# Kernel optimization log

Hardware: AMD Instinct MI355X
Metric: run time of the kernel (lower is better)

Reference implementation:

```python
import jax, jax.numpy as jnp
import numpy as np

B, L, N, H, D, TOPK = 32, 720, 512, 16, 64, 8
TEMP = 1.0


def setup_inputs() -> dict:
    key = jax.random.key(0)
    ks = jax.random.split(key, 18)
    s = lambda k, shp, fan: jax.random.normal(k, shp, jnp.float32) / np.sqrt(fan)
    return {
        'x': jax.random.normal(ks[0], (B, L, N), jnp.float32),
        'var_embed': s(ks[1], (N, H), H),
        'Wq': s(ks[2], (H, H), H), 'bq': jnp.zeros((H,), jnp.float32),
        'Wk': s(ks[3], (H, H), H), 'bk': jnp.zeros((H,), jnp.float32),
        'Wscore': s(ks[4], (N, 1), N), 'bscore': jnp.zeros((1,), jnp.float32),
        'Wc1': s(ks[5], (N, D), N), 'bc1': jnp.zeros((D,), jnp.float32),
        'Wc2': s(ks[6], (D, D), D), 'bc2': jnp.zeros((D,), jnp.float32),
        'Wcn': s(ks[7], (D, N), D), 'bcn': jnp.zeros((N,), jnp.float32),
        'Wg': s(ks[8], (2 * N, N), 2 * N), 'bg': jnp.zeros((N,), jnp.float32),
        'Wf': s(ks[9], (N, N), N), 'bf': jnp.zeros((N,), jnp.float32),
        'gamma': jnp.ones((N,), jnp.float32), 'beta': jnp.zeros((N,), jnp.float32),
    }


def _forward(x, var_embed, Wq, bq, Wk, bk, Wscore, bscore, Wc1, bc1, Wc2, bc2,
             Wcn, bcn, Wg, bg, Wf, bf, gamma, beta):
    # --- SparseVariableRouter (eval mode: no gumbel noise) ---
    Q = var_embed @ Wq + bq          # [N,H]
    K = var_embed @ Wk + bk          # [N,H]
    sim = Q @ K.T                    # [N,N] (identical across batch in torch)
    eye = jnp.eye(N, dtype=bool)
    sim = jnp.where(eye, -1e9, sim)
    topk_vals, topk_idx = jax.lax.top_k(sim, TOPK)      # [N,k]
    w = jax.nn.softmax(topk_vals / TEMP, axis=-1)        # [N,k]
    x_perm = jnp.transpose(x, (0, 2, 1))                 # [B,N,L]
    neighbors = x_perm[:, topk_idx, :]                   # [B,N,k,L] gather
    ring_out = jnp.einsum('bnkl,nk->bln', neighbors, w)  # [B,L,N]
    # --- center path ---
    attn = jax.nn.softmax(x @ Wscore + bscore, axis=1)   # [B,L,1] softmax over L
    center_raw = jnp.sum(x * attn, axis=1)               # [B,N]
    c = jax.nn.gelu(center_raw @ Wc1 + bc1, approximate=False)
    c = jax.nn.gelu(c @ Wc2 + bc2, approximate=False)
    center = c @ Wcn + bcn                               # [B,N]
    center_b = jnp.broadcast_to(center[:, None, :], (x.shape[0], x.shape[1], N))
    # --- gated fusion + residual LN ---
    gate = jax.nn.sigmoid(jnp.concatenate([ring_out, center_b], axis=-1) @ Wg + bg)
    fused = gate * ring_out + (1.0 - gate) * center_b
    fused = fused @ Wf + bf
    h = fused + x
    mu = jnp.mean(h, axis=-1, keepdims=True)
    var = jnp.var(h, axis=-1, keepdims=True)
    return (h - mu) * jax.lax.rsqrt(var + 1e-5) * gamma + beta


def reference(x, var_embed, Wq, bq, Wk, bk, Wscore, bscore, Wc1, bc1, Wc2, bc2,
              Wcn, bcn, Wg, bg, Wf, bf, gamma, beta):
    return _forward(x, var_embed, Wq, bq, Wk, bk, Wscore, bscore, Wc1, bc1,
                    Wc2, bc2, Wcn, bcn, Wg, bg, Wf, bf, gamma, beta)
```

## Files before the change

kernel.cpp:

```cpp
#include <hip/hip_runtime.h>
#include <hip/hip_bf16.h>
#include <math.h>

#define B_ 32
#define L_ 720
#define N_ 512
#define H_ 16
#define D_ 64
#define TOPK_ 8
#define M_ (B_ * L_)
#define RPB 8
#define CRCH 16
#define CRL (L_ / CRCH)
#define OROWS 64

typedef __bf16 bf16x8 __attribute__((ext_vector_type(8)));
typedef float f32x16 __attribute__((ext_vector_type(16)));

__device__ __forceinline__ void async_cp16(const __hip_bfloat16* g, __hip_bfloat16* l) {
    __builtin_amdgcn_global_load_lds(
        (const __attribute__((address_space(1))) void*)g,
        (__attribute__((address_space(3))) void*)l, 16, 0, 0);
}

__device__ __forceinline__ bf16x8 frag_ld(const __hip_bfloat16* base, int row, int j0) {
    return *(const bf16x8*)(base + row * 64 + (((j0) ^ (row & 7)) << 3));
}

__device__ __forceinline__ f32x16 fzero16() {
    f32x16 z;
    #pragma unroll
    for (int e = 0; e < 16; ++e) z[e] = 0.f;
    return z;
}

__global__ __launch_bounds__(512) void prep_kernel(
    const float* __restrict__ Wg, const float* __restrict__ Wf,
    __hip_bfloat16* __restrict__ WgT, __hip_bfloat16* __restrict__ WfT,
    const float* __restrict__ ve,
    const float* __restrict__ Wq, const float* __restrict__ bq,
    const float* __restrict__ Wk, const float* __restrict__ bk,
    float* __restrict__ Qm, float* __restrict__ Km)
{
    const int bx = blockIdx.x;
    if (bx < 512) {
        const int n = bx;
        const int k = threadIdx.x;
        WgT[n * N_ + k] = __float2bfloat16(Wg[(size_t)k * N_ + n]);
        WfT[n * N_ + k] = __float2bfloat16(Wf[(size_t)k * N_ + n]);
    } else {
        const int g = (bx - 512) * 512 + threadIdx.x;
        const int j = g >> 4, h = g & 15;
        const float* vr = ve + j * H_;
        float q = bq[h], k = bk[h];
        #pragma unroll
        for (int m = 0; m < H_; ++m) {
            const float v = vr[m];
            q += v * Wq[m * H_ + h];
            k += v * Wk[m * H_ + h];
        }
        Qm[g] = q;
        Km[g] = k;
    }
}

__global__ __launch_bounds__(64) void topk_kernel(
    const float* __restrict__ Qm, const float* __restrict__ Km,
    float* __restrict__ w_out, int* __restrict__ idx_out)
{
    const int n = blockIdx.x;
    const int lane = threadIdx.x;

    float4 q0, q1, q2, q3;
    {
        const float4* qr = (const float4*)(Qm + n * H_);
        q0 = qr[0]; q1 = qr[1]; q2 = qr[2]; q3 = qr[3];
    }

    float sv[8]; int si[8];
    #pragma unroll
    for (int c = 0; c < 8; ++c) {
        const int j = c * 64 + lane;
        const float4* kr = (const float4*)(Km + j * H_);
        float4 k0 = kr[0], k1 = kr[1], k2 = kr[2], k3 = kr[3];
        float s = q0.x * k0.x + q0.y * k0.y + q0.z * k0.z + q0.w * k0.w
                + q1.x * k1.x + q1.y * k1.y + q1.z * k1.z + q1.w * k1.w
                + q2.x * k2.x + q2.y * k2.y + q2.z * k2.z + q2.w * k2.w
                + q3.x * k3.x + q3.y * k3.y + q3.z * k3.z + q3.w * k3.w;
        sv[c] = (j == n) ? -1e9f : s;
        si[c] = j;
    }

    float keepv[TOPK_]; int keepi[TOPK_];
    #pragma unroll
    for (int k = 0; k < TOPK_; ++k) {
        float bv = sv[0]; int bi = si[0]; int bslot = 0;
        #pragma unroll
        for (int c = 1; c < 8; ++c)
            if (sv[c] > bv || (sv[c] == bv && si[c] < bi)) { bv = sv[c]; bi = si[c]; bslot = c; }
        float v = bv; int i = bi;
        #pragma unroll
        for (int off = 32; off > 0; off >>= 1) {
            float v2 = __shfl_xor(v, off);
            int   i2 = __shfl_xor(i, off);
            if (v2 > v || (v2 == v && i2 < i)) { v = v2; i = i2; }
        }
        keepv[k] = v; keepi[k] = i;
        if (i == bi) sv[bslot] = -INFINITY;
    }

    if (lane == 0) {
        float vmax = keepv[0];
        float ev[TOPK_], esum = 0.f;
        #pragma unroll
        for (int k = 0; k < TOPK_; k++) { ev[k] = expf(keepv[k] - vmax); esum += ev[k]; }
        float inv = 1.f / esum;
        #pragma unroll
        for (int k = 0; k < TOPK_; k++) {
            w_out[n * TOPK_ + k] = ev[k] * inv;
            idx_out[n * TOPK_ + k] = keepi[k];
        }
    }
}

__global__ __launch_bounds__(512) void ring_kernel(
    const float* __restrict__ x, const float* __restrict__ w,
    const int* __restrict__ idx,
    const float* __restrict__ Wscore, const float* __restrict__ bscore,
    __hip_bfloat16* __restrict__ ring, float* __restrict__ s)
{
    __shared__ float xs[RPB][N_];
    __shared__ float wsh[N_ * TOPK_];
    __shared__ int   ish[N_ * TOPK_];
    const int t = threadIdx.x;
    const int row0 = blockIdx.x * RPB;

    for (int i = t; i < N_ * TOPK_; i += 512) { wsh[i] = w[i]; ish[i] = idx[i]; }
    {
        const float4* xg = (const float4*)(x + (size_t)row0 * N_);
        float4* xsf = (float4*)&xs[0][0];
        xsf[t] = xg[t];
        xsf[t + 512] = xg[t + 512];
    }
    __syncthreads();

    {
        const int wv = t >> 6, lane = t & 63;
        float sa = 0.f;
        #pragma unroll
        for (int i = 0; i < 8; ++i) sa += xs[wv][lane + i * 64] * Wscore[lane + i * 64];
        for (int off = 32; off > 0; off >>= 1) sa += __shfl_down(sa, off);
        if (lane == 0) s[row0 + wv] = sa + bscore[0];
    }

    float wr[TOPK_]; int ir[TOPK_];
    #pragma unroll
    for (int k = 0; k < TOPK_; ++k) { wr[k] = wsh[t * TOPK_ + k]; ir[k] = ish[t * TOPK_ + k]; }
    #pragma unroll
    for (int r = 0; r < RPB; ++r) {
        float acc = 0.f;
        #pragma unroll
        for (int k = 0; k < TOPK_; ++k) acc += wr[k] * xs[r][ir[k]];
        ring[(size_t)(row0 + r) * N_ + t] = __float2bfloat16(acc);
    }
}

__global__ __launch_bounds__(512) void center_raw_kernel(
    const float* __restrict__ x, const float* __restrict__ s,
    float* __restrict__ craw_p)
{
    const int b = blockIdx.x >> 4;
    const int c = blockIdx.x & 15;
    const int n = threadIdx.x;
    __shared__ float red[8];
    __shared__ float ash[CRL];
    const float* srow = s + (size_t)b * L_;

    float lmax = -1e30f;
    for (int l = n; l < L_; l += 512) lmax = fmaxf(lmax, srow[l]);
    for (int off = 32; off > 0; off >>= 1) lmax = fmaxf(lmax, __shfl_down(lmax, off));
    if ((n & 63) == 0) red[n >> 6] = lmax;
    __syncthreads();
    float gmax = red[0];
    #pragma unroll
    for (int w = 1; w < 8; ++w) gmax = fmaxf(gmax, red[w]);
    __syncthreads();

    float lsum = 0.f;
    for (int l = n; l < L_; l += 512) lsum += expf(srow[l] - gmax);
    for (int off = 32; off > 0; off >>= 1) lsum += __shfl_down(lsum, off);
    if ((n & 63) == 0) red[n >> 6] = lsum;
    __syncthreads();
    float tsum = 0.f;
    #pragma unroll
    for (int w = 0; w < 8; ++w) tsum += red[w];
    const float inv = 1.f / tsum;

    const int l0 = c * CRL;
    if (n < CRL) ash[n] = expf(srow[l0 + n] - gmax) * inv;
    __syncthreads();

    const float* xb = x + ((size_t)b * L_ + l0) * N_;
    float acc = 0.f;
    #pragma unroll 3
    for (int l = 0; l < CRL; l++) acc += ash[l] * xb[(size_t)l * N_ + n];
    craw_p[(size_t)(b * CRCH + c) * N_ + n] = acc;
}

__device__ __forceinline__ float gelu_exact(float v) {
    return 0.5f * v * (1.0f + erff(v * 0.70710678118654752440f));
}

__global__ __launch_bounds__(512) void center_mlp_kernel(
    const float* __restrict__ craw_p,
    const float* __restrict__ Wc1, const float* __restrict__ bc1,
    const float* __restrict__ Wc2, const float* __restrict__ bc2,
    const float* __restrict__ Wcn, const float* __restrict__ bcn,
    const float* __restrict__ Wg,  const float* __restrict__ bg,
    float* __restrict__ center, float* __restrict__ cg)
{
    const int b = blockIdx.x;
    const int t = threadIdx.x;
    const int col = t & 63;
    const int seg = t >> 6;
    __shared__ float cr[N_];
    __shared__ float psum[8][D_];
    __shared__ float h1[D_];
    __shared__ float h2[D_];

    {
        float acc = 0.f;
        #pragma unroll
        for (int c = 0; c < CRCH; ++c) acc += craw_p[(size_t)(b * CRCH + c) * N_ + t];
        cr[t] = acc;
    }
    __syncthreads();
    {
        float p = 0.f;
        #pragma unroll 8
        for (int m = seg * 64; m < seg * 64 + 64; ++m) p += cr[m] * Wc1[m * D_ + col];
        psum[seg][col] = p;
    }
    __syncthreads();
    if (t < D_) {
        float acc = bc1[t];
        #pragma unroll
        for (int s2 = 0; s2 < 8; ++s2) acc += psum[s2][t];
        h1[t] = gelu_exact(acc);
    }
    __syncthreads();
    if (t < D_) {
        float acc = bc2[t];
        #pragma unroll 8
        for (int j = 0; j < D_; j++) acc += h1[j] * Wc2[j * D_ + t];
        h2[t] = gelu_exact(acc);
    }
    __syncthreads();
    float centv;
    {
        float acc = bcn[t];
        #pragma unroll 8
        for (int j = 0; j < D_; j++) acc += h2[j] * Wcn[j * N_ + t];
        centv = acc;
        center[b * N_ + t] = acc;
    }
    __syncthreads();
    cr[t] = centv;
    __syncthreads();
    {
        float acc = bg[t];
        const float* wp = Wg + (size_t)N_ * N_ + t;
        #pragma unroll 8
        for (int m = 0; m < N_; ++m) { acc += cr[m] * wp[0]; wp += N_; }
        cg[b * N_ + t] = acc;
    }
}

#define GEMM_BODY(EPILOGUE)                                                    \
    __shared__ __hip_bfloat16 Ash[64 * 64];                                    \
    __shared__ __hip_bfloat16 Bsh[64 * 64];                                    \
    const int tid  = threadIdx.x;                                              \
    const int lane = tid & 63;                                                 \
    const int wv   = tid >> 6;                                                 \
    const int m32  = lane & 31;                                                \
    const int half = lane >> 5;                                                \
    const int wr   = wv >> 1;                                                  \
    const int wc   = wv & 1;                                                   \
    const int row0 = blockIdx.x * 64;                                          \
    const int n0   = blockIdx.y * 64;                                          \
    const int swz  = (lane & 7) ^ (lane >> 3);                                 \
    const int rln  = lane >> 3;                                                \
    f32x16 acc;                                                                \
    _Pragma("unroll") for (int e = 0; e < 16; e++) acc[e] = 0.f;               \
    for (int step = 0; step < 8; ++step) {                                     \
        const int k0 = step * 64;                                              \
        const __hip_bfloat16* Ab = A  + (size_t)row0 * N_ + k0 + swz * 8;      \
        const __hip_bfloat16* Bb = BT + (size_t)n0   * N_ + k0 + swz * 8;      \
        __syncthreads();                                                       \
        _Pragma("unroll") for (int j = 0; j < 2; ++j) {                        \
            const int r = j * 32 + wv * 8 + rln;                               \
            const int lb = (j * 256 + wv * 64) * 8;                            \
            async_cp16(Ab + (size_t)r * N_, Ash + lb);                         \
            async_cp16(Bb + (size_t)r * N_, Bsh + lb);                         \
        }                                                                      \
        __syncthreads();                                                       \
        _Pragma("unroll") for (int ks = 0; ks < 4; ++ks) {                     \
            const int j0 = ks * 2 + half;                                      \
            bf16x8 a0 = frag_ld(Ash, wr * 32 + m32, j0);                       \
            bf16x8 b0 = frag_ld(Bsh, wc * 32 + m32, j0);                       \
            acc = __builtin_amdgcn_mfma_f32_32x32x16_bf16(a0, b0, acc, 0, 0, 0); \
        }                                                                      \
    }                                                                          \
    _Pragma("unroll") for (int reg = 0; reg < 16; ++reg) {                     \
        const int rg  = row0 + wr * 32 +                                       \
                        (reg & 3) + 8 * (reg >> 2) + 4 * half;                 \
        const int col = n0 + wc * 32 + m32;                                    \
        const float aval = acc[reg];                                           \
        EPILOGUE                                                               \
    }

__global__ __launch_bounds__(256) void gemm_gate_kernel(
    const __hip_bfloat16* __restrict__ A,
    const __hip_bfloat16* __restrict__ BT,
    const float* __restrict__ cg,
    const float* __restrict__ center,
    __hip_bfloat16* __restrict__ fused)
{
    GEMM_BODY({
        const int bbase = row0 / L_;
        const int b = (rg >= (bbase + 1) * L_) ? bbase + 1 : bbase;
        const float logit = aval + cg[b * N_ + col];
        const float g = 1.f / (1.f + expf(-logit));
        const float rv = __bfloat162float(A[(size_t)rg * N_ + col]);
        const float f = g * rv + (1.f - g) * center[b * N_ + col];
        fused[(size_t)rg * N_ + col] = __float2bfloat16(f);
    })
}

__global__ __launch_bounds__(512) void gemm_out_ln_kernel(
    const __hip_bfloat16* __restrict__ A,
    const __hip_bfloat16* __restrict__ BT,
    const float* __restrict__ x,
    const float* __restrict__ bfv,
    const float* __restrict__ gamma,
    const float* __restrict__ beta,
    float* __restrict__ out)
{
    __shared__ __hip_bfloat16 Wsh[512 * 64];
    __shared__ __hip_bfloat16 Dsh[64 * 64];
    __shared__ float ps[8][2][32];
    __shared__ float pq[8][2][32];

    const int tid  = threadIdx.x;
    const int lane = tid & 63;
    const int wv8  = tid >> 6;
    const int m32  = lane & 31;
    const int half = lane >> 5;
    const int row0 = blockIdx.x * OROWS;
    const int swz  = (lane & 7) ^ (lane >> 3);
    const int rln  = lane >> 3;

    f32x16 acc[2][2];
    #pragma unroll
    for (int g = 0; g < 2; ++g)
        #pragma unroll
        for (int i = 0; i < 2; ++i) acc[g][i] = fzero16();

    for (int step = 0; step < 8; ++step) {
        const int k0 = step * 64;
        __syncthreads();
        #pragma unroll
        for (int j = 0; j < 8; ++j) {
            const int r = j * 64 + wv8 * 8 + rln;
            async_cp16(BT + (size_t)r * N_ + k0 + swz * 8,
                       Wsh + (j * 512 + wv8 * 64) * 8);
        }
        {
            const int r = wv8 * 8 + rln;
            async_cp16(A + (size_t)(row0 + r) * N_ + k0 + swz * 8,
                       Dsh + (wv8 * 64) * 8);
        }
        __syncthreads();
        #pragma unroll
        for (int ks = 0; ks < 4; ++ks) {
            const int j0 = ks * 2 + half;
            bf16x8 d0 = frag_ld(Dsh, m32, j0);
            bf16x8 d1 = frag_ld(Dsh, 32 + m32, j0);
            bf16x8 wa = frag_ld(Wsh, (wv8 * 2 + 0) * 32 + m32, j0);
            bf16x8 wb = frag_ld(Wsh, (wv8 * 2 + 1) * 32 + m32, j0);
            acc[0][0] = __builtin_amdgcn_mfma_f32_32x32x16_bf16(wa, d0, acc[0][0], 0, 0, 0);
            acc[0][1] = __builtin_amdgcn_mfma_f32_32x32x16_bf16(wb, d0, acc[0][1], 0, 0, 0);
            acc[1][0] = __builtin_amdgcn_mfma_f32_32x32x16_bf16(wa, d1, acc[1][0], 0, 0, 0);
            acc[1][1] = __builtin_amdgcn_mfma_f32_32x32x16_bf16(wb, d1, acc[1][1], 0, 0, 0);
        }
    }

    float ls[2] = {0.f, 0.f};
    float lq[2] = {0.f, 0.f};
    #pragma unroll
    for (int g = 0; g < 2; ++g) {
        const int rowg = row0 + g * 32 + m32;
        #pragma unroll
        for (int i = 0; i < 2; ++i) {
            const int ntb = (wv8 * 2 + i) * 32;
            #pragma unroll
            for (int q = 0; q < 4; ++q) {
                const int nb = ntb + 8 * q + 4 * half;
                const float4 bq = *(const float4*)(bfv + nb);
                const float4 xq = *(const float4*)(x + (size_t)rowg * N_ + nb);
                float v0 = acc[g][i][4 * q + 0] + bq.x + xq.x;
                float v1 = acc[g][i][4 * q + 1] + bq.y + xq.y;
                float v2 = acc[g][i][4 * q + 2] + bq.z + xq.z;
                float v3 = acc[g][i][4 * q + 3] + bq.w + xq.w;
                acc[g][i][4 * q + 0] = v0;
                acc[g][i][4 * q + 1] = v1;
                acc[g][i][4 * q + 2] = v2;
                acc[g][i][4 * q + 3] = v3;
                ls[g] += v0 + v1 + v2 + v3;
                lq[g] += v0 * v0 + v1 * v1 + v2 * v2 + v3 * v3;
            }
        }
    }

    #pragma unroll
    for (int g = 0; g < 2; ++g) {
        ls[g] += __shfl_xor(ls[g], 32);
        lq[g] += __shfl_xor(lq[g], 32);
    }
    if (half == 0) {
        ps[wv8][0][m32] = ls[0]; pq[wv8][0][m32] = lq[0];
        ps[wv8][1][m32] = ls[1]; pq[wv8][1][m32] = lq[1];
    }
    __syncthreads();

    #pragma unroll
    for (int g = 0; g < 2; ++g) {
        float S = 0.f, Q2 = 0.f;
        #pragma unroll
        for (int w = 0; w < 8; ++w) { S += ps[w][g][m32]; Q2 += pq[w][g][m32]; }
        const float mu  = S * (1.0f / N_);
        const float var = Q2 * (1.0f / N_) - mu * mu;
        const float inv = rsqrtf(var + 1e-5f);
        const int rowg = row0 + g * 32 + m32;
        #pragma unroll
        for (int i = 0; i < 2; ++i) {
            const int ntb = (wv8 * 2 + i) * 32;
            #pragma unroll
            for (int q = 0; q < 4; ++q) {
                const int nb = ntb + 8 * q + 4 * half;
                const float4 g4 = *(const float4*)(gamma + nb);
                const float4 b4 = *(const float4*)(beta + nb);
                float4 o;
                o.x = (acc[g][i][4 * q + 0] - mu) * inv * g4.x + b4.x;
                o.y = (acc[g][i][4 * q + 1] - mu) * inv * g4.y + b4.y;
                o.z = (acc[g][i][4 * q + 2] - mu) * inv * g4.z + b4.z;
                o.w = (acc[g][i][4 * q + 3] - mu) * inv * g4.w + b4.w;
                *(float4*)(out + (size_t)rowg * N_ + nb) = o;
            }
        }
    }
}

extern "C" void kernel_launch(void* const* d_in, const int* in_sizes, int n_in,
                              void* d_out, int out_size, void* d_ws, size_t ws_size,
                              hipStream_t stream) {
    const float* x       = (const float*)d_in[0];
    const float* ve      = (const float*)d_in[1];
    const float* Wq      = (const float*)d_in[2];
    const float* bq      = (const float*)d_in[3];
    const float* Wk      = (const float*)d_in[4];
    const float* bk      = (const float*)d_in[5];
    const float* Wscore  = (const float*)d_in[6];
    const float* bscore  = (const float*)d_in[7];
    const float* Wc1     = (const float*)d_in[8];
    const float* bc1     = (const float*)d_in[9];
    const float* Wc2     = (const float*)d_in[10];
    const float* bc2     = (const float*)d_in[11];
    const float* Wcn     = (const float*)d_in[12];
    const float* bcn     = (const float*)d_in[13];
    const float* Wg      = (const float*)d_in[14];
    const float* bg      = (const float*)d_in[15];
    const float* Wf      = (const float*)d_in[16];
    const float* bf      = (const float*)d_in[17];
    const float* gamma   = (const float*)d_in[18];
    const float* beta    = (const float*)d_in[19];
    float* out = (float*)d_out;

    char* p = (char*)d_ws;
    float* ws_w    = (float*)p; p += N_ * TOPK_ * sizeof(float);
    int*   ws_idx  = (int*)p;   p += N_ * TOPK_ * sizeof(int);
    float* ws_s    = (float*)p; p += B_ * L_ * sizeof(float);
    float* ws_crp  = (float*)p; p += B_ * CRCH * N_ * sizeof(float);
    float* ws_cent = (float*)p; p += B_ * N_ * sizeof(float);
    float* ws_cg   = (float*)p; p += B_ * N_ * sizeof(float);
    float* ws_Q    = (float*)p; p += N_ * H_ * sizeof(float);
    float* ws_K    = (float*)p; p += N_ * H_ * sizeof(float);
    __hip_bfloat16* ws_ring  = (__hip_bfloat16*)p; p += (size_t)M_ * N_ * sizeof(__hip_bfloat16);
    __hip_bfloat16* ws_fused = (__hip_bfloat16*)p; p += (size_t)M_ * N_ * sizeof(__hip_bfloat16);
    __hip_bfloat16* ws_WgT   = (__hip_bfloat16*)p; p += (size_t)N_ * N_ * sizeof(__hip_bfloat16);
    __hip_bfloat16* ws_WfT   = (__hip_bfloat16*)p; p += (size_t)N_ * N_ * sizeof(__hip_bfloat16);

    prep_kernel<<<528, 512, 0, stream>>>(Wg, Wf, ws_WgT, ws_WfT,
                                         ve, Wq, bq, Wk, bk, ws_Q, ws_K);
    topk_kernel<<<N_, 64, 0, stream>>>(ws_Q, ws_K, ws_w, ws_idx);
    ring_kernel<<<M_ / RPB, 512, 0, stream>>>(x, ws_w, ws_idx, Wscore, bscore,
                                              ws_ring, ws_s);
    center_raw_kernel<<<B_ * CRCH, 512, 0, stream>>>(x, ws_s, ws_crp);
    center_mlp_kernel<<<B_, 512, 0, stream>>>(ws_crp, Wc1, bc1, Wc2, bc2,
                                              Wcn, bcn, Wg, bg, ws_cent, ws_cg);
    dim3 ggrid(M_ / 64, N_ / 64);
    gemm_gate_kernel<<<ggrid, 256, 0, stream>>>(ws_ring, ws_WgT, ws_cg,
                                                ws_cent, ws_fused);
    gemm_out_ln_kernel<<<M_ / OROWS, 512, 0, stream>>>(ws_fused, ws_WfT, x, bf,
                                                       gamma, beta, out);
}
```

Before: 277.9 us.

## Read Wf from MFMA-packed global layout and split center-gate GEMV across blocks

The output GEMM+LayerNorm kernel stops staging the full 512x64 Wf tile in LDS each K-step. Wf is pre-packed into the per-lane MFMA fragment order, so each wave loads its B fragments straight from global/L2, and only the activation tile is staged, double-buffered in LDS. Rows per block drop to 32, which shrinks LDS use and doubles the grid. The center-gate GEMV over Wg's lower half moves out of the 32-block MLP kernel into a separate kernel spread over 8x32 blocks, adding one launch in exchange for more parallelism.

```diff
diff --git a/kernel.cpp b/kernel.cpp
--- a/kernel.cpp
+++ b/kernel.cpp
@@ -12,7 +12,7 @@
 #define RPB 8
 #define CRCH 16
 #define CRL (L_ / CRCH)
-#define OROWS 64
+#define OROWS 32
 
 typedef __bf16 bf16x8 __attribute__((ext_vector_type(8)));
 typedef float f32x16 __attribute__((ext_vector_type(16)));
@@ -36,7 +36,7 @@
 
 __global__ __launch_bounds__(512) void prep_kernel(
     const float* __restrict__ Wg, const float* __restrict__ Wf,
-    __hip_bfloat16* __restrict__ WgT, __hip_bfloat16* __restrict__ WfT,
+    __hip_bfloat16* __restrict__ WgT, __hip_bfloat16* __restrict__ WfPk,
     const float* __restrict__ ve,
     const float* __restrict__ Wq, const float* __restrict__ bq,
     const float* __restrict__ Wk, const float* __restrict__ bk,
@@ -47,7 +47,11 @@
         const int n = bx;
         const int k = threadIdx.x;
         WgT[n * N_ + k] = __float2bfloat16(Wg[(size_t)k * N_ + n]);
-        WfT[n * N_ + k] = __float2bfloat16(Wf[(size_t)k * N_ + n]);
+        const int cblk = n >> 5;
+        const int ks32 = k >> 4;
+        const int l    = (n & 31) + 32 * ((k >> 3) & 1);
+        WfPk[(((size_t)cblk * 32 + ks32) * 64 + l) * 8 + (k & 7)] =
+            __float2bfloat16(Wf[(size_t)k * N_ + n]);
     } else {
         const int g = (bx - 512) * 512 + threadIdx.x;
         const int j = g >> 4, h = g & 15;
@@ -216,8 +220,7 @@
     const float* __restrict__ Wc1, const float* __restrict__ bc1,
     const float* __restrict__ Wc2, const float* __restrict__ bc2,
     const float* __restrict__ Wcn, const float* __restrict__ bcn,
-    const float* __restrict__ Wg,  const float* __restrict__ bg,
-    float* __restrict__ center, float* __restrict__ cg)
+    float* __restrict__ center)
 {
     const int b = blockIdx.x;
     const int t = threadIdx.x;
@@ -256,23 +259,41 @@
         h2[t] = gelu_exact(acc);
     }
     __syncthreads();
-    float centv;
     {
         float acc = bcn[t];
         #pragma unroll 8
         for (int j = 0; j < D_; j++) acc += h2[j] * Wcn[j * N_ + t];
-        centv = acc;
         center[b * N_ + t] = acc;
     }
-    __syncthreads();
-    cr[t] = centv;
-    __syncthreads();
-    {
-        float acc = bg[t];
-        const float* wp = Wg + (size_t)N_ * N_ + t;
+}
+
+__global__ __launch_bounds__(512) void cg_kernel(
+    const float* __restrict__ center, const float* __restrict__ Wg,
+    const float* __restrict__ bg, float* __restrict__ cg)
+{
+    const int nc = blockIdx.x;
+    const int b  = blockIdx.y;
+    const int t  = threadIdx.x;
+    const int col = nc * 64 + (t & 63);
+    const int seg = t >> 6;
+    __shared__ float cs[N_];
+    __shared__ float psum[8][64];
+
+    cs[t] = center[b * N_ + t];
+    __syncthreads();
+    {
+        float p = 0.f;
+        const float* wp = Wg + (size_t)(N_ + seg * 64) * N_ + col;
         #pragma unroll 8
-        for (int m = 0; m < N_; ++m) { acc += cr[m] * wp[0]; wp += N_; }
-        cg[b * N_ + t] = acc;
+        for (int m = 0; m < 64; ++m) { p += cs[seg * 64 + m] * wp[0]; wp += N_; }
+        psum[seg][t & 63] = p;
+    }
+    __syncthreads();
+    if (t < 64) {
+        float acc = bg[nc * 64 + t];
+        #pragma unroll
+        for (int s2 = 0; s2 < 8; ++s2) acc += psum[s2][t];
+        cg[b * N_ + nc * 64 + t] = acc;
     }
 }
 
@@ -339,17 +360,16 @@
 
 __global__ __launch_bounds__(512) void gemm_out_ln_kernel(
     const __hip_bfloat16* __restrict__ A,
-    const __hip_bfloat16* __restrict__ BT,
+    const __hip_bfloat16* __restrict__ Wpk,
     const float* __restrict__ x,
     const float* __restrict__ bfv,
     const float* __restrict__ gamma,
     const float* __restrict__ beta,
     float* __restrict__ out)
 {
-    __shared__ __hip_bfloat16 Wsh[512 * 64];
-    __shared__ __hip_bfloat16 Dsh[64 * 64];
-    __shared__ float ps[8][2][32];
-    __shared__ float pq[8][2][32];
+    __shared__ __hip_bfloat16 Dsh[2][32 * 64];
+    __shared__ float ps[8][32];
+    __shared__ float pq[8][32];
 
     const int tid  = threadIdx.x;
     const int lane = tid & 63;
@@ -360,105 +380,83 @@
     const int swz  = (lane & 7) ^ (lane >> 3);
     const int rln  = lane >> 3;
 
-    f32x16 acc[2][2];
-    #pragma unroll
-    for (int g = 0; g < 2; ++g)
-        #pragma unroll
-        for (int i = 0; i < 2; ++i) acc[g][i] = fzero16();
-
+    f32x16 acc0 = fzero16();
+    f32x16 acc1 = fzero16();
+    const __hip_bfloat16* wbase = Wpk + ((size_t)(wv8 * 2) * 32 * 64 + lane) * 8;
+
+    if (wv8 < 4) {
+        const int r = wv8 * 8 + rln;
+        async_cp16(A + (size_t)(row0 + r) * N_ + swz * 8, &Dsh[0][(wv8 * 64) * 8]);
+    }
+    __syncthreads();
     for (int step = 0; step < 8; ++step) {
-        const int k0 = step * 64;
-        __syncthreads();
-        #pragma unroll
-        for (int j = 0; j < 8; ++j) {
-            const int r = j * 64 + wv8 * 8 + rln;
-            async_cp16(BT + (size_t)r * N_ + k0 + swz * 8,
-                       Wsh + (j * 512 + wv8 * 64) * 8);
+        const int cur = step & 1;
+        if (step < 7 && wv8 < 4) {
+            const int r = wv8 * 8 + rln;
+            async_cp16(A + (size_t)(row0 + r) * N_ + (step + 1) * 64 + swz * 8,
+                       &Dsh[cur ^ 1][(wv8 * 64) * 8]);
         }
-        {
-            const int r = wv8 * 8 + rln;
-            async_cp16(A + (size_t)(row0 + r) * N_ + k0 + swz * 8,
-                       Dsh + (wv8 * 64) * 8);
+        #pragma unroll
+        for (int ks = 0; ks < 4; ++ks) {
+            const int j0   = ks * 2 + half;
+            const int ks32 = step * 4 + ks;
+            bf16x8 d0 = frag_ld(Dsh[cur], m32, j0);
+            bf16x8 wa = *(const bf16x8*)(wbase + (size_t)ks32 * 64 * 8);
+            bf16x8 wb = *(const bf16x8*)(wbase + (size_t)(32 * 64 + ks32 * 64) * 8);
+            acc0 = __builtin_amdgcn_mfma_f32_32x32x16_bf16(wa, d0, acc0, 0, 0, 0);
+            acc1 = __builtin_amdgcn_mfma_f32_32x32x16_bf16(wb, d0, acc1, 0, 0, 0);
         }
         __syncthreads();
-        #pragma unroll
-        for (int ks = 0; ks < 4; ++ks) {
-            const int j0 = ks * 2 + half;
-            bf16x8 d0 = frag_ld(Dsh, m32, j0);
-            bf16x8 d1 = frag_ld(Dsh, 32 + m32, j0);
-            bf16x8 wa = frag_ld(Wsh, (wv8 * 2 + 0) * 32 + m32, j0);
-            bf16x8 wb = frag_ld(Wsh, (wv8 * 2 + 1) * 32 + m32, j0);
-            acc[0][0] = __builtin_amdgcn_mfma_f32_32x32x16_bf16(wa, d0, acc[0][0], 0, 0, 0);
-            acc[0][1] = __builtin_amdgcn_mfma_f32_32x32x16_bf16(wb, d0, acc[0][1], 0, 0, 0);
-            acc[1][0] = __builtin_amdgcn_mfma_f32_32x32x16_bf16(wa, d1, acc[1][0], 0, 0, 0);
-            acc[1][1] = __builtin_amdgcn_mfma_f32_32x32x16_bf16(wb, d1, acc[1][1], 0, 0, 0);
-        }
-    }
-
-    float ls[2] = {0.f, 0.f};
-    float lq[2] = {0.f, 0.f};
-    #pragma unroll
-    for (int g = 0; g < 2; ++g) {
-        const int rowg = row0 + g * 32 + m32;
-        #pragma unroll
-        for (int i = 0; i < 2; ++i) {
-            const int ntb = (wv8 * 2 + i) * 32;
-            #pragma unroll
-            for (int q = 0; q < 4; ++q) {
-                const int nb = ntb + 8 * q + 4 * half;
-                const float4 bq = *(const float4*)(bfv + nb);
-                const float4 xq = *(const float4*)(x + (size_t)rowg * N_ + nb);
-                float v0 = acc[g][i][4 * q + 0] + bq.x + xq.x;
-                float v1 = acc[g][i][4 * q + 1] + bq.y + xq.y;
-                float v2 = acc[g][i][4 * q + 2] + bq.z + xq.z;
-                float v3 = acc[g][i][4 * q + 3] + bq.w + xq.w;
-                acc[g][i][4 * q + 0] = v0;
-                acc[g][i][4 * q + 1] = v1;
-                acc[g][i][4 * q + 2] = v2;
-                acc[g][i][4 * q + 3] = v3;
-                ls[g] += v0 + v1 + v2 + v3;
-                lq[g] += v0 * v0 + v1 * v1 + v2 * v2 + v3 * v3;
-            }
-        }
-    }
-
-    #pragma unroll
-    for (int g = 0; g < 2; ++g) {
-        ls[g] += __shfl_xor(ls[g], 32);
-        lq[g] += __shfl_xor(lq[g], 32);
-    }
-    if (half == 0) {
-        ps[wv8][0][m32] = ls[0]; pq[wv8][0][m32] = lq[0];
-        ps[wv8][1][m32] = ls[1]; pq[wv8][1][m32] = lq[1];
-    }
-    __syncthreads();
-
-    #pragma unroll
-    for (int g = 0; g < 2; ++g) {
-        float S = 0.f, Q2 = 0.f;
-        #pragma unroll
-        for (int w = 0; w < 8; ++w) { S += ps[w][g][m32]; Q2 += pq[w][g][m32]; }
-        const float mu  = S * (1.0f / N_);
-        const float var = Q2 * (1.0f / N_) - mu * mu;
-        const float inv = rsqrtf(var + 1e-5f);
-        const int rowg = row0 + g * 32 + m32;
-        #pragma unroll
-        for (int i = 0; i < 2; ++i) {
-            const int ntb = (wv8 * 2 + i) * 32;
-            #pragma unroll
-            for (int q = 0; q < 4; ++q) {
-                const int nb = ntb + 8 * q + 4 * half;
-                const float4 g4 = *(const float4*)(gamma + nb);
-                const float4 b4 = *(const float4*)(beta + nb);
-                float4 o;
-                o.x = (acc[g][i][4 * q + 0] - mu) * inv * g4.x + b4.x;
-                o.y = (acc[g][i][4 * q + 1] - mu) * inv * g4.y + b4.y;
-                o.z = (acc[g][i][4 * q + 2] - mu) * inv * g4.z + b4.z;
-                o.w = (acc[g][i][4 * q + 3] - mu) * inv * g4.w + b4.w;
-                *(float4*)(out + (size_t)rowg * N_ + nb) = o;
-            }
-        }
-    }
+    }
+
+    const int rowg = row0 + m32;
+    float ls = 0.f, lq = 0.f;
+#define OEPI2(AC, I)                                                           \
+    {                                                                          \
+        const int ntb = (wv8 * 2 + (I)) * 32;                                  \
+        _Pragma("unroll") for (int q = 0; q < 4; ++q) {                        \
+            const int nb = ntb + 8 * q + 4 * half;                             \
+            const float4 bq = *(const float4*)(bfv + nb);                      \
+            const float4 xq = *(const float4*)(x + (size_t)rowg * N_ + nb);    \
+            AC[4 * q + 0] += bq.x + xq.x;                                      \
+            AC[4 * q + 1] += bq.y + xq.y;                                      \
+            AC[4 * q + 2] += bq.z + xq.z;                                      \
+            AC[4 * q + 3] += bq.w + xq.w;                                      \
+            ls += AC[4 * q + 0] + AC[4 * q + 1] + AC[4 * q + 2] + AC[4 * q + 3]; \
+            lq += AC[4 * q + 0] * AC[4 * q + 0] + AC[4 * q + 1] * AC[4 * q + 1]  \
+                + AC[4 * q + 2] * AC[4 * q + 2] + AC[4 * q + 3] * AC[4 * q + 3]; \
+        }                                                                      \
+    }
+    OEPI2(acc0, 0) OEPI2(acc1, 1)
+
+    ls += __shfl_xor(ls, 32);
+    lq += __shfl_xor(lq, 32);
+    if (half == 0) { ps[wv8][m32] = ls; pq[wv8][m32] = lq; }
+    __syncthreads();
+
+    float S = 0.f, Q2 = 0.f;
+    #pragma unroll
+    for (int w = 0; w < 8; ++w) { S += ps[w][m32]; Q2 += pq[w][m32]; }
+    const float mu  = S * (1.0f / N_);
+    const float var = Q2 * (1.0f / N_) - mu * mu;
+    const float inv = rsqrtf(var + 1e-5f);
+
+#define LSTORE2(AC, I)                                                         \
+    {                                                                          \
+        const int ntb = (wv8 * 2 + (I)) * 32;                                  \
+        _Pragma("unroll") for (int q = 0; q < 4; ++q) {                        \
+            const int nb = ntb + 8 * q + 4 * half;                             \
+            const float4 g4 = *(const float4*)(gamma + nb);                    \
+            const float4 b4 = *(const float4*)(beta + nb);                     \
+            float4 o;                                                          \
+            o.x = (AC[4 * q + 0] - mu) * inv * g4.x + b4.x;                    \
+            o.y = (AC[4 * q + 1] - mu) * inv * g4.y + b4.y;                    \
+            o.z = (AC[4 * q + 2] - mu) * inv * g4.z + b4.z;                    \
+            o.w = (AC[4 * q + 3] - mu) * inv * g4.w + b4.w;                    \
+            *(float4*)(out + (size_t)rowg * N_ + nb) = o;                      \
+        }                                                                      \
+    }
+    LSTORE2(acc0, 0) LSTORE2(acc1, 1)
 }
 
 extern "C" void kernel_launch(void* const* d_in, const int* in_sizes, int n_in,
@@ -498,19 +496,20 @@
     __hip_bfloat16* ws_ring  = (__hip_bfloat16*)p; p += (size_t)M_ * N_ * sizeof(__hip_bfloat16);
     __hip_bfloat16* ws_fused = (__hip_bfloat16*)p; p += (size_t)M_ * N_ * sizeof(__hip_bfloat16);
     __hip_bfloat16* ws_WgT   = (__hip_bfloat16*)p; p += (size_t)N_ * N_ * sizeof(__hip_bfloat16);
-    __hip_bfloat16* ws_WfT   = (__hip_bfloat16*)p; p += (size_t)N_ * N_ * sizeof(__hip_bfloat16);
-
-    prep_kernel<<<528, 512, 0, stream>>>(Wg, Wf, ws_WgT, ws_WfT,
+    __hip_bfloat16* ws_WfPk  = (__hip_bfloat16*)p; p += (size_t)N_ * N_ * sizeof(__hip_bfloat16);
+
+    prep_kernel<<<528, 512, 0, stream>>>(Wg, Wf, ws_WgT, ws_WfPk,
                                          ve, Wq, bq, Wk, bk, ws_Q, ws_K);
     topk_kernel<<<N_, 64, 0, stream>>>(ws_Q, ws_K, ws_w, ws_idx);
     ring_kernel<<<M_ / RPB, 512, 0, stream>>>(x, ws_w, ws_idx, Wscore, bscore,
                                               ws_ring, ws_s);
     center_raw_kernel<<<B_ * CRCH, 512, 0, stream>>>(x, ws_s, ws_crp);
     center_mlp_kernel<<<B_, 512, 0, stream>>>(ws_crp, Wc1, bc1, Wc2, bc2,
-                                              Wcn, bcn, Wg, bg, ws_cent, ws_cg);
+                                              Wcn, bcn, ws_cent);
+    cg_kernel<<<dim3(8, B_), 512, 0, stream>>>(ws_cent, Wg, bg, ws_cg);
     dim3 ggrid(M_ / 64, N_ / 64);
     gemm_gate_kernel<<<ggrid, 256, 0, stream>>>(ws_ring, ws_WgT, ws_cg,
                                                 ws_cent, ws_fused);
-    gemm_out_ln_kernel<<<M_ / OROWS, 512, 0, stream>>>(ws_fused, ws_WfT, x, bf,
+    gemm_out_ln_kernel<<<M_ / OROWS, 512, 0, stream>>>(ws_fused, ws_WfPk, x, bf,
                                                        gamma, beta, out);
 }
```

Measured after the change: 252.9 us. 9.0% less time.
